# Optimization experiments

Hardware: AMD Instinct MI355X
Metric: run time of the kernel (lower is better)

The kernel has to match this reference:

```python
import jax, jax.numpy as jnp
import numpy as np

N = 50000      # nodes
D = 128        # feature dim
NNZ = 800000   # edges (avg degree 16)
M = 30         # Chebyshev order

def setup_inputs() -> dict:
    key = jax.random.key(0)
    k1, k2, k3, k4, k5 = jax.random.split(key, 5)
    rows = jax.random.randint(k1, (NNZ,), 0, N)
    cols = jax.random.randint(k2, (NNZ,), 0, N)
    # scale so row sums (Gershgorin bound on spectral radius) stay ~< 1,
    # mimicking a rescaled Laplacian required for a stable Chebyshev recurrence
    vals = jax.random.uniform(k3, (NNZ,), dtype=jnp.float32) * (0.5 / 16.0)
    X = jax.random.normal(k4, (N, D), dtype=jnp.float32)
    coeffs = jax.random.normal(k5, (M,), dtype=jnp.float32)
    return {"rows": rows, "cols": cols, "vals": vals, "X": X, "coeffs": coeffs}

def _spmm(rows, cols, vals, X, n):
    # y[r] += vals[e] * X[c]  for each edge e=(r,c): sparse L @ X
    return jax.ops.segment_sum(vals[:, None] * X[cols], rows, num_segments=n)

def reference(rows, cols, vals, X, coeffs):
    n = X.shape[0]
    T0 = X                                   # T_0 = X
    T1 = _spmm(rows, cols, vals, X, n)       # T_1 = L @ X
    acc = coeffs[0] * T0 + coeffs[1] * T1
    def step(carry, ck):
        T0, T1, acc = carry
        Tk = 2.0 * _spmm(rows, cols, vals, T1, n) - T0   # T_k = 2 L T_{k-1} - T_{k-2}
        return (T1, Tk, acc + ck * Tk), None
    (_, _, acc), _ = jax.lax.scan(step, (T0, T1, acc), coeffs[2:])
    return acc
```

## Files before the change

kernel.cpp:

```cpp
#include <hip/hip_runtime.h>
#include <hip/hip_fp16.h>

#define FD 128
#define WPB 4
#define RPW 2


__global__ void zero_i32(int* __restrict__ p, int n) {
  int i = blockIdx.x * blockDim.x + threadIdx.x;
  if (i < n) p[i] = 0;
}

__global__ void hist_kernel(const int* __restrict__ rows, int* __restrict__ cnt, int nnz) {
  int i = blockIdx.x * blockDim.x + threadIdx.x;
  if (i < nnz) atomicAdd(&cnt[rows[i]], 1);
}

__global__ void block_reduce(const int* __restrict__ cnt, int* __restrict__ bsum, int n) {
  __shared__ int sm[256];
  int i = blockIdx.x * 256 + threadIdx.x;
  sm[threadIdx.x] = (i < n) ? cnt[i] : 0;
  __syncthreads();
  for (int off = 128; off > 0; off >>= 1) {
    if (threadIdx.x < off) sm[threadIdx.x] += sm[threadIdx.x + off];
    __syncthreads();
  }
  if (threadIdx.x == 0) bsum[blockIdx.x] = sm[0];
}

__global__ void scan_bsum(const int* __restrict__ bsum, int* __restrict__ bpre, int nb) {
  __shared__ int sm[1024];
  const int tid = threadIdx.x;
  sm[tid] = (tid < nb) ? bsum[tid] : 0;
  __syncthreads();
  for (int off = 1; off < 1024; off <<= 1) {
    int t = (tid >= off) ? sm[tid - off] : 0;
    __syncthreads();
    sm[tid] += t;
    __syncthreads();
  }
  if (tid < nb) bpre[tid] = (tid == 0) ? 0 : sm[tid - 1];
}

__global__ void block_scan(const int* __restrict__ cnt, const int* __restrict__ bpre,
                           int* __restrict__ row_ptr, int n) {
  __shared__ int sm[256];
  const int tid = threadIdx.x;
  int i = blockIdx.x * 256 + tid;
  sm[tid] = (i < n) ? cnt[i] : 0;
  __syncthreads();
  for (int off = 1; off < 256; off <<= 1) {
    int t = (tid >= off) ? sm[tid - off] : 0;
    __syncthreads();
    sm[tid] += t;
    __syncthreads();
  }
  if (i < n) row_ptr[i + 1] = sm[tid] + bpre[blockIdx.x];
  if (i == 0) row_ptr[0] = 0;
}

__global__ void copy_i32(const int* __restrict__ src, int* __restrict__ dst, int n) {
  int i = blockIdx.x * blockDim.x + threadIdx.x;
  if (i < n) dst[i] = src[i];
}

__global__ void scatter_kernel(const int* __restrict__ rows, const int* __restrict__ cols,
                               const float* __restrict__ vals, int* __restrict__ fill,
                               int2* __restrict__ pk, int nnz) {
  int i = blockIdx.x * blockDim.x + threadIdx.x;
  if (i < nnz) {
    int r = rows[i];
    int pos = atomicAdd(&fill[r], 1);
    pk[pos] = make_int2(cols[i] << 7, __float_as_int(vals[i]));
  }
}

__global__ void f32_to_f16_f8(const float* __restrict__ src, __half* __restrict__ dst,
                              unsigned int* __restrict__ dst8, int n4) {
  int i = blockIdx.x * blockDim.x + threadIdx.x;
  if (i < n4) {
    float4 v = ((const float4*)src)[i];
    __half2* d = (__half2*)dst + 2 * (size_t)i;
    d[0] = __floats2half2_rn(v.x, v.y);
    d[1] = __floats2half2_rn(v.z, v.w);
    int w = 0;
    w = __builtin_amdgcn_cvt_pk_fp8_f32(v.x, v.y, w, false);
    w = __builtin_amdgcn_cvt_pk_fp8_f32(v.z, v.w, w, true);
    dst8[i] = (unsigned int)w;
  }
}


typedef float v2f __attribute__((ext_vector_type(2)));

__device__ __forceinline__ void consume16(uint4 raw, float v, float acc[16]) {
  v2f f;
  f = __builtin_amdgcn_cvt_pk_f32_fp8((int)raw.x, false);
  acc[0] = fmaf(v, f.x, acc[0]);  acc[1] = fmaf(v, f.y, acc[1]);
  f = __builtin_amdgcn_cvt_pk_f32_fp8((int)raw.x, true);
  acc[2] = fmaf(v, f.x, acc[2]);  acc[3] = fmaf(v, f.y, acc[3]);
  f = __builtin_amdgcn_cvt_pk_f32_fp8((int)raw.y, false);
  acc[4] = fmaf(v, f.x, acc[4]);  acc[5] = fmaf(v, f.y, acc[5]);
  f = __builtin_amdgcn_cvt_pk_f32_fp8((int)raw.y, true);
  acc[6] = fmaf(v, f.x, acc[6]);  acc[7] = fmaf(v, f.y, acc[7]);
  f = __builtin_amdgcn_cvt_pk_f32_fp8((int)raw.z, false);
  acc[8] = fmaf(v, f.x, acc[8]);  acc[9] = fmaf(v, f.y, acc[9]);
  f = __builtin_amdgcn_cvt_pk_f32_fp8((int)raw.z, true);
  acc[10] = fmaf(v, f.x, acc[10]); acc[11] = fmaf(v, f.y, acc[11]);
  f = __builtin_amdgcn_cvt_pk_f32_fp8((int)raw.w, false);
  acc[12] = fmaf(v, f.x, acc[12]); acc[13] = fmaf(v, f.y, acc[13]);
  f = __builtin_amdgcn_cvt_pk_f32_fp8((int)raw.w, true);
  acc[14] = fmaf(v, f.x, acc[14]); acc[15] = fmaf(v, f.y, acc[15]);
}

__device__ __forceinline__ void gather_rows(const int2* __restrict__ pk,
                                            const char* __restrict__ Tfl,
                                            int e, int end, int sub4,
                                            float acc[16]) {
  while (__any(e < end)) {
    const int el = max(end - 1, 0);
    const int i0 = e + sub4, i1 = e + 4 + sub4, i2 = e + 8 + sub4, i3 = e + 12 + sub4;
    int2 cv0 = pk[min(i0, el)];
    int2 cv1 = pk[min(i1, el)];
    int2 cv2 = pk[min(i2, el)];
    int2 cv3 = pk[min(i3, el)];
    uint4 w0 = *(const uint4*)(Tfl + cv0.x);
    uint4 w1 = *(const uint4*)(Tfl + cv1.x);
    uint4 w2 = *(const uint4*)(Tfl + cv2.x);
    uint4 w3 = *(const uint4*)(Tfl + cv3.x);
    float v0 = (i0 < end) ? __int_as_float(cv0.y) : 0.f;
    float v1 = (i1 < end) ? __int_as_float(cv1.y) : 0.f;
    float v2 = (i2 < end) ? __int_as_float(cv2.y) : 0.f;
    float v3 = (i3 < end) ? __int_as_float(cv3.y) : 0.f;
    consume16(w0, v0, acc);
    consume16(w1, v1, acc);
    consume16(w2, v2, acc);
    consume16(w3, v3, acc);
    e += 16;
  }
}

__device__ __forceinline__ void reduce_subs(float acc[16]) {
#pragma unroll
  for (int j = 0; j < 16; ++j) {
    acc[j] += __shfl_xor(acc[j], 8, 64);
    acc[j] += __shfl_xor(acc[j], 16, 64);
  }
}


__global__ __launch_bounds__(256) void clen_step(
    const int* __restrict__ rp, const int2* __restrict__ pk,
    const unsigned char* __restrict__ src8, const __half* __restrict__ Xh, __half* pd,
    unsigned char* __restrict__ dst8,
    const float* __restrict__ coeffs, int k, int flags, int M, int n) {
  const int lane = threadIdx.x & 63;
  const int halfw = lane >> 5;
  const int sub4 = (lane >> 3) & 3;
  const int fl = lane & 7;
  const int wid = threadIdx.x >> 6;
  const int wbase = blockIdx.x * (WPB * RPW) + wid * RPW;
  if (wbase >= n) return;
  const int r = wbase + halfw;
  const bool rok = (r < n);
  const int rv = rok ? r : (n - 1);

  int e = rp[rv];
  int end = rok ? rp[rv + 1] : e;
  const char* Tfl = (const char*)src8 + fl * 16;

  float acc[16];
#pragma unroll
  for (int j = 0; j < 16; ++j) acc[j] = 0.f;
  gather_rows(pk, Tfl, e, end, sub4, acc);
  reduce_subs(acc);

  if (sub4 == 0 && rok) {
    float ck = coeffs[k];
    if (flags & 2) ck -= coeffs[M - 1];
    const float g2 = (flags & 4) ? 2.f * coeffs[M - 1] : 2.f;
    const uint4* Xr = (const uint4*)(Xh + (size_t)r * FD);
    uint4 xr0 = Xr[fl * 2], xr1 = Xr[fl * 2 + 1];
    uint4 pr0 = make_uint4(0,0,0,0), pr1 = make_uint4(0,0,0,0);
    if (flags & 1) {
      const uint4* Pr = (const uint4*)(pd + (size_t)r * FD);
      pr0 = Pr[fl * 2]; pr1 = Pr[fl * 2 + 1];
    }
    const __half2* xh0 = (const __half2*)&xr0;
    const __half2* xh1 = (const __half2*)&xr1;
    const __half2* ph0 = (const __half2*)&pr0;
    const __half2* ph1 = (const __half2*)&pr1;
    float t[16];
#pragma unroll
    for (int q = 0; q < 4; ++q) {
      float2 x = __half22float2(xh0[q]);
      float2 p = (flags & 1) ? __half22float2(ph0[q]) : make_float2(0.f, 0.f);
      t[2*q]   = fmaf(g2, acc[2*q],   fmaf(ck, x.x, -p.x));
      t[2*q+1] = fmaf(g2, acc[2*q+1], fmaf(ck, x.y, -p.y));
    }
#pragma unroll
    for (int q = 0; q < 4; ++q) {
      float2 x = __half22float2(xh1[q]);
      float2 p = (flags & 1) ? __half22float2(ph1[q]) : make_float2(0.f, 0.f);
      t[8+2*q]   = fmaf(g2, acc[8+2*q],   fmaf(ck, x.x, -p.x));
      t[8+2*q+1] = fmaf(g2, acc[8+2*q+1], fmaf(ck, x.y, -p.y));
    }
    uint4 o0, o1;
    __half2* oh0 = (__half2*)&o0;
    __half2* oh1 = (__half2*)&o1;
#pragma unroll
    for (int q = 0; q < 4; ++q) {
      oh0[q] = __floats2half2_rn(t[2*q], t[2*q+1]);
      oh1[q] = __floats2half2_rn(t[8+2*q], t[8+2*q+1]);
    }
    ((uint4*)(pd + (size_t)r * FD))[fl * 2] = o0;
    ((uint4*)(pd + (size_t)r * FD))[fl * 2 + 1] = o1;
    uint4 m8;
    int w;
    w = 0;
    w = __builtin_amdgcn_cvt_pk_fp8_f32(t[0], t[1], w, false);
    w = __builtin_amdgcn_cvt_pk_fp8_f32(t[2], t[3], w, true);
    m8.x = (unsigned int)w;
    w = 0;
    w = __builtin_amdgcn_cvt_pk_fp8_f32(t[4], t[5], w, false);
    w = __builtin_amdgcn_cvt_pk_fp8_f32(t[6], t[7], w, true);
    m8.y = (unsigned int)w;
    w = 0;
    w = __builtin_amdgcn_cvt_pk_fp8_f32(t[8], t[9], w, false);
    w = __builtin_amdgcn_cvt_pk_fp8_f32(t[10], t[11], w, true);
    m8.z = (unsigned int)w;
    w = 0;
    w = __builtin_amdgcn_cvt_pk_fp8_f32(t[12], t[13], w, false);
    w = __builtin_amdgcn_cvt_pk_fp8_f32(t[14], t[15], w, true);
    m8.w = (unsigned int)w;
    ((uint4*)(dst8 + (size_t)r * FD))[fl] = m8;
  }
}

__global__ __launch_bounds__(256) void clen_final(
    const int* __restrict__ rp, const int2* __restrict__ pk,
    const unsigned char* __restrict__ b18, const __half* __restrict__ b2,
    const float* __restrict__ X, float* __restrict__ out,
    const float* __restrict__ coeffs, int n) {
  const int lane = threadIdx.x & 63;
  const int halfw = lane >> 5;
  const int sub4 = (lane >> 3) & 3;
  const int fl = lane & 7;
  const int wid = threadIdx.x >> 6;
  const int wbase = blockIdx.x * (WPB * RPW) + wid * RPW;
  if (wbase >= n) return;
  const int r = wbase + halfw;
  const bool rok = (r < n);
  const int rv = rok ? r : (n - 1);

  int e = rp[rv];
  int end = rok ? rp[rv + 1] : e;
  const char* Tfl = (const char*)b18 + fl * 16;

  float acc[16];
#pragma unroll
  for (int j = 0; j < 16; ++j) acc[j] = 0.f;
  gather_rows(pk, Tfl, e, end, sub4, acc);
  reduce_subs(acc);

  if (sub4 == 0 && rok) {
    const float c0 = coeffs[0];
    const uint4* Br = (const uint4*)(b2 + (size_t)r * FD);
    uint4 pr0 = Br[fl * 2], pr1 = Br[fl * 2 + 1];
    const float4* Xr = (const float4*)(X + (size_t)r * FD);
    float4 x0 = Xr[fl * 4], x1 = Xr[fl * 4 + 1], x2 = Xr[fl * 4 + 2], x3 = Xr[fl * 4 + 3];
    const __half2* ph0 = (const __half2*)&pr0;
    const __half2* ph1 = (const __half2*)&pr1;
    float p[16];
#pragma unroll
    for (int q = 0; q < 4; ++q) {
      float2 a = __half22float2(ph0[q]);
      p[2*q] = a.x; p[2*q+1] = a.y;
      float2 b = __half22float2(ph1[q]);
      p[8+2*q] = b.x; p[8+2*q+1] = b.y;
    }
    float4 o0, o1, o2, o3;
    o0.x = fmaf(c0, x0.x, acc[0] - p[0]);
    o0.y = fmaf(c0, x0.y, acc[1] - p[1]);
    o0.z = fmaf(c0, x0.z, acc[2] - p[2]);
    o0.w = fmaf(c0, x0.w, acc[3] - p[3]);
    o1.x = fmaf(c0, x1.x, acc[4] - p[4]);
    o1.y = fmaf(c0, x1.y, acc[5] - p[5]);
    o1.z = fmaf(c0, x1.z, acc[6] - p[6]);
    o1.w = fmaf(c0, x1.w, acc[7] - p[7]);
    o2.x = fmaf(c0, x2.x, acc[8] - p[8]);
    o2.y = fmaf(c0, x2.y, acc[9] - p[9]);
    o2.z = fmaf(c0, x2.z, acc[10] - p[10]);
    o2.w = fmaf(c0, x2.w, acc[11] - p[11]);
    o3.x = fmaf(c0, x3.x, acc[12] - p[12]);
    o3.y = fmaf(c0, x3.y, acc[13] - p[13]);
    o3.z = fmaf(c0, x3.z, acc[14] - p[14]);
    o3.w = fmaf(c0, x3.w, acc[15] - p[15]);
    float4* Or = (float4*)(out + (size_t)r * FD);
    Or[fl * 4] = o0; Or[fl * 4 + 1] = o1; Or[fl * 4 + 2] = o2; Or[fl * 4 + 3] = o3;
  }
}


extern "C" void kernel_launch(void* const* d_in, const int* in_sizes, int n_in,
                              void* d_out, int out_size, void* d_ws, size_t ws_size,
                              hipStream_t stream) {
  const int* rows = (const int*)d_in[0];
  const int* cols = (const int*)d_in[1];
  const float* vals = (const float*)d_in[2];
  const float* X = (const float*)d_in[3];
  const float* coeffs = (const float*)d_in[4];
  float* out = (float*)d_out;

  const int nnz = in_sizes[0];
  const int n = in_sizes[3] / FD;
  const int M = in_sizes[4];

  auto align_up = [](size_t x) { return (x + 255) & ~(size_t)255; };
  char* w = (char*)d_ws;
  size_t off = 0;
  int* row_ptr = (int*)(w + off); off = align_up(off + (size_t)(n + 1) * 4);
  int* row_fill = (int*)(w + off); off = align_up(off + (size_t)n * 4);
  int* bsum = (int*)(w + off); off = align_up(off + 1024 * 4);
  int* bpre = (int*)(w + off); off = align_up(off + 1024 * 4);
  int2* pk = (int2*)(w + off); off = align_up(off + (size_t)nnz * 8);
  __half* Xh = (__half*)(w + off); off = align_up(off + (size_t)n * FD * 2);
  __half* buf0 = (__half*)(w + off); off = align_up(off + (size_t)n * FD * 2);
  __half* buf1 = (__half*)(w + off); off = align_up(off + (size_t)n * FD * 2);
  unsigned char* m80 = (unsigned char*)(w + off); off = align_up(off + (size_t)n * FD);
  unsigned char* m81 = (unsigned char*)(w + off); off = align_up(off + (size_t)n * FD);
  __half* bufs[2] = {buf0, buf1};
  unsigned char* m8[2] = {m80, m81};
  (void)ws_size;

  const int B = 256;
  const int gN = (n + B - 1) / B;
  const int gE = (nnz + B - 1) / B;
  const int gS = (n + WPB * RPW - 1) / (WPB * RPW);
  const int n4 = n * FD / 4;
  const int gC = (n4 + B - 1) / B;

  zero_i32<<<gN, B, 0, stream>>>(row_fill, n);
  hist_kernel<<<gE, B, 0, stream>>>(rows, row_fill, nnz);
  block_reduce<<<gN, B, 0, stream>>>(row_fill, bsum, n);
  scan_bsum<<<1, 1024, 0, stream>>>(bsum, bpre, gN);
  block_scan<<<gN, B, 0, stream>>>(row_fill, bpre, row_ptr, n);
  copy_i32<<<gN, B, 0, stream>>>(row_ptr, row_fill, n);
  scatter_kernel<<<gE, B, 0, stream>>>(rows, cols, vals, row_fill, pk, nnz);
  f32_to_f16_f8<<<gC, B, 0, stream>>>(X, Xh, (unsigned int*)m8[(M - 1) & 1], n4);

  clen_step<<<gS, B, 0, stream>>>(row_ptr, pk, m8[(M - 1) & 1], Xh, bufs[(M - 2) & 1],
                                  m8[(M - 2) & 1], coeffs, M - 2, 4, M, n);
  clen_step<<<gS, B, 0, stream>>>(row_ptr, pk, m8[(M - 2) & 1], Xh, bufs[(M - 3) & 1],
                                  m8[(M - 3) & 1], coeffs, M - 3, 2, M, n);
  for (int k = M - 4; k >= 1; --k) {
    clen_step<<<gS, B, 0, stream>>>(row_ptr, pk, m8[(k + 1) & 1], Xh, bufs[k & 1],
                                    m8[k & 1], coeffs, k, 1, M, n);
  }
  clen_final<<<gS, B, 0, stream>>>(row_ptr, pk, m8[1], bufs[0], X, out, coeffs, n);
}
```

Measured before the change: 938.5 us.

## Window scatter passes by row range and prefetch epilogue rows with nontemporal access

The CSR scatter now runs in 8 passes over the edge list. Each pass only places edges whose row falls in one eighth of the node range, so the atomics and writes to the packed edge array stay inside a smaller, cache-friendly window. The cost is reading rows[] eight times. In the step and final kernels, the per-row X and previous-buffer loads are issued before the gather so their latency overlaps it. These loads and the output stores now use nontemporal hints to avoid polluting the cache used by the fp8 gather table.

```diff
diff --git a/kernel.cpp b/kernel.cpp
--- a/kernel.cpp
+++ b/kernel.cpp
@@ -4,6 +4,7 @@
 #define FD 128
 #define WPB 4
 #define RPW 2
+#define SCPASS 8
 
 
 __global__ void zero_i32(int* __restrict__ p, int n) {
@@ -66,10 +67,15 @@
 
 __global__ void scatter_kernel(const int* __restrict__ rows, const int* __restrict__ cols,
                                const float* __restrict__ vals, int* __restrict__ fill,
-                               int2* __restrict__ pk, int nnz) {
-  int i = blockIdx.x * blockDim.x + threadIdx.x;
-  if (i < nnz) {
-    int r = rows[i];
+                               int2* __restrict__ pk, int nnz, int n, int gE) {
+  const int p = blockIdx.x / gE;
+  const int chunk = blockIdx.x - p * gE;
+  const int i = chunk * blockDim.x + threadIdx.x;
+  if (i >= nnz) return;
+  const int r = rows[i];
+  const int wlo = (int)(((long long)p * n) >> 3);
+  const int whi = (int)(((long long)(p + 1) * n) >> 3);
+  if (r >= wlo && r < whi) {
     int pos = atomicAdd(&fill[r], 1);
     pk[pos] = make_int2(cols[i] << 7, __float_as_int(vals[i]));
   }
@@ -88,6 +94,27 @@
     w = __builtin_amdgcn_cvt_pk_fp8_f32(v.z, v.w, w, true);
     dst8[i] = (unsigned int)w;
   }
+}
+
+
+typedef unsigned int v4u __attribute__((ext_vector_type(4)));
+typedef float v4f __attribute__((ext_vector_type(4)));
+
+__device__ __forceinline__ uint4 nt_ld_u4(const uint4* p) {
+  v4u v = __builtin_nontemporal_load((const v4u*)p);
+  return make_uint4(v.x, v.y, v.z, v.w);
+}
+__device__ __forceinline__ float4 nt_ld_f4(const float4* p) {
+  v4f v = __builtin_nontemporal_load((const v4f*)p);
+  return make_float4(v.x, v.y, v.z, v.w);
+}
+__device__ __forceinline__ void nt_st_u4(uint4* p, uint4 x) {
+  v4u v = {x.x, x.y, x.z, x.w};
+  __builtin_nontemporal_store(v, (v4u*)p);
+}
+__device__ __forceinline__ void nt_st_f4(float4* p, float4 x) {
+  v4f v = {x.x, x.y, x.z, x.w};
+  __builtin_nontemporal_store(v, (v4f*)p);
 }
 
 
@@ -169,6 +196,19 @@
   int end = rok ? rp[rv + 1] : e;
   const char* Tfl = (const char*)src8 + fl * 16;
 
+  uint4 xr0 = make_uint4(0,0,0,0), xr1 = make_uint4(0,0,0,0);
+  uint4 pr0 = make_uint4(0,0,0,0), pr1 = make_uint4(0,0,0,0);
+  if (sub4 == 0 && rok) {
+    const uint4* Xr = (const uint4*)(Xh + (size_t)r * FD);
+    xr0 = nt_ld_u4(Xr + fl * 2);
+    xr1 = nt_ld_u4(Xr + fl * 2 + 1);
+    if (flags & 1) {
+      const uint4* Pr = (const uint4*)(pd + (size_t)r * FD);
+      pr0 = nt_ld_u4(Pr + fl * 2);
+      pr1 = nt_ld_u4(Pr + fl * 2 + 1);
+    }
+  }
+
   float acc[16];
 #pragma unroll
   for (int j = 0; j < 16; ++j) acc[j] = 0.f;
@@ -179,13 +219,6 @@
     float ck = coeffs[k];
     if (flags & 2) ck -= coeffs[M - 1];
     const float g2 = (flags & 4) ? 2.f * coeffs[M - 1] : 2.f;
-    const uint4* Xr = (const uint4*)(Xh + (size_t)r * FD);
-    uint4 xr0 = Xr[fl * 2], xr1 = Xr[fl * 2 + 1];
-    uint4 pr0 = make_uint4(0,0,0,0), pr1 = make_uint4(0,0,0,0);
-    if (flags & 1) {
-      const uint4* Pr = (const uint4*)(pd + (size_t)r * FD);
-      pr0 = Pr[fl * 2]; pr1 = Pr[fl * 2 + 1];
-    }
     const __half2* xh0 = (const __half2*)&xr0;
     const __half2* xh1 = (const __half2*)&xr1;
     const __half2* ph0 = (const __half2*)&pr0;
@@ -213,8 +246,8 @@
       oh0[q] = __floats2half2_rn(t[2*q], t[2*q+1]);
       oh1[q] = __floats2half2_rn(t[8+2*q], t[8+2*q+1]);
     }
-    ((uint4*)(pd + (size_t)r * FD))[fl * 2] = o0;
-    ((uint4*)(pd + (size_t)r * FD))[fl * 2 + 1] = o1;
+    nt_st_u4((uint4*)(pd + (size_t)r * FD) + fl * 2, o0);
+    nt_st_u4((uint4*)(pd + (size_t)r * FD) + fl * 2 + 1, o1);
     uint4 m8;
     int w;
     w = 0;
@@ -257,6 +290,20 @@
   int end = rok ? rp[rv + 1] : e;
   const char* Tfl = (const char*)b18 + fl * 16;
 
+  uint4 pr0 = make_uint4(0,0,0,0), pr1 = make_uint4(0,0,0,0);
+  float4 x0 = make_float4(0.f,0.f,0.f,0.f), x1 = make_float4(0.f,0.f,0.f,0.f);
+  float4 x2 = make_float4(0.f,0.f,0.f,0.f), x3 = make_float4(0.f,0.f,0.f,0.f);
+  if (sub4 == 0 && rok) {
+    const uint4* Br = (const uint4*)(b2 + (size_t)r * FD);
+    pr0 = nt_ld_u4(Br + fl * 2);
+    pr1 = nt_ld_u4(Br + fl * 2 + 1);
+    const float4* Xr = (const float4*)(X + (size_t)r * FD);
+    x0 = nt_ld_f4(Xr + fl * 4);
+    x1 = nt_ld_f4(Xr + fl * 4 + 1);
+    x2 = nt_ld_f4(Xr + fl * 4 + 2);
+    x3 = nt_ld_f4(Xr + fl * 4 + 3);
+  }
+
   float acc[16];
 #pragma unroll
   for (int j = 0; j < 16; ++j) acc[j] = 0.f;
@@ -265,10 +312,6 @@
 
   if (sub4 == 0 && rok) {
     const float c0 = coeffs[0];
-    const uint4* Br = (const uint4*)(b2 + (size_t)r * FD);
-    uint4 pr0 = Br[fl * 2], pr1 = Br[fl * 2 + 1];
-    const float4* Xr = (const float4*)(X + (size_t)r * FD);
-    float4 x0 = Xr[fl * 4], x1 = Xr[fl * 4 + 1], x2 = Xr[fl * 4 + 2], x3 = Xr[fl * 4 + 3];
     const __half2* ph0 = (const __half2*)&pr0;
     const __half2* ph1 = (const __half2*)&pr1;
     float p[16];
@@ -297,7 +340,10 @@
     o3.z = fmaf(c0, x3.z, acc[14] - p[14]);
     o3.w = fmaf(c0, x3.w, acc[15] - p[15]);
     float4* Or = (float4*)(out + (size_t)r * FD);
-    Or[fl * 4] = o0; Or[fl * 4 + 1] = o1; Or[fl * 4 + 2] = o2; Or[fl * 4 + 3] = o3;
+    nt_st_f4(Or + fl * 4, o0);
+    nt_st_f4(Or + fl * 4 + 1, o1);
+    nt_st_f4(Or + fl * 4 + 2, o2);
+    nt_st_f4(Or + fl * 4 + 3, o3);
   }
 }
 
@@ -346,7 +392,7 @@
   scan_bsum<<<1, 1024, 0, stream>>>(bsum, bpre, gN);
   block_scan<<<gN, B, 0, stream>>>(row_fill, bpre, row_ptr, n);
   copy_i32<<<gN, B, 0, stream>>>(row_ptr, row_fill, n);
-  scatter_kernel<<<gE, B, 0, stream>>>(rows, cols, vals, row_fill, pk, nnz);
+  scatter_kernel<<<gE * SCPASS, B, 0, stream>>>(rows, cols, vals, row_fill, pk, nnz, n, gE);
   f32_to_f16_f8<<<gC, B, 0, stream>>>(X, Xh, (unsigned int*)m8[(M - 1) & 1], n4);
 
   clen_step<<<gS, B, 0, stream>>>(row_ptr, pk, m8[(M - 1) & 1], Xh, bufs[(M - 2) & 1],
```

New measurement: 1.104 ms. +17.7%, slower.
